# Performance work log

Hardware: AMD Instinct MI355X
Metric: run time of the kernel (lower is better)

Reference implementation:

```python
import jax, jax.numpy as jnp
import numpy as np

N, E, R = 50000, 1600000, 8
IN_F, HID_F, OUT_F = 128, 64, 64


def setup_inputs() -> dict:
    key = jax.random.key(0)
    ks = jax.random.split(key, 9)
    x = jax.random.normal(ks[0], (N, IN_F), dtype=jnp.float32)
    edge_index = jax.random.randint(ks[1], (2, E), 0, N, dtype=jnp.int64)
    edge_type = jax.random.randint(ks[2], (E,), 0, R, dtype=jnp.int64)
    # layer 1 params (scaled like glorot)
    s1 = 1.0 / np.sqrt(IN_F)
    W1_rel = jax.random.normal(ks[3], (R, IN_F, HID_F), dtype=jnp.float32) * s1
    W1_root = jax.random.normal(ks[4], (IN_F, HID_F), dtype=jnp.float32) * s1
    b1 = jnp.zeros((HID_F,), dtype=jnp.float32)
    # layer 2 params
    s2 = 1.0 / np.sqrt(HID_F)
    W2_rel = jax.random.normal(ks[5], (R, HID_F, OUT_F), dtype=jnp.float32) * s2
    W2_root = jax.random.normal(ks[6], (HID_F, OUT_F), dtype=jnp.float32) * s2
    b2 = jnp.zeros((OUT_F,), dtype=jnp.float32)
    return {"x": x, "edge_index": edge_index, "edge_type": edge_type,
            "W1_rel": W1_rel, "W1_root": W1_root, "b1": b1,
            "W2_rel": W2_rel, "W2_root": W2_root, "b2": b2}


def _rgcn_conv(x, src, dst, etype, W_rel, W_root, b):
    """PyG RGCNConv: root transform + per-relation mean-aggregated messages."""
    n = x.shape[0]
    r = W_rel.shape[0]
    # per-relation transform of all node features: [R, N, H]
    xw = jnp.einsum('nd,rdh->rnh', x, W_rel)
    # per-edge message: transformed source feature under the edge's relation
    msg = xw[etype, src]  # [E, H]
    # mean normalization per (dst, relation) pair
    key = dst * r + etype  # [E]
    cnt = jax.ops.segment_sum(jnp.ones(etype.shape, dtype=x.dtype), key,
                              num_segments=n * r)
    inv = 1.0 / jnp.maximum(cnt, 1.0)
    msg = msg * inv[key][:, None]
    # scatter-add into target nodes
    agg = jax.ops.segment_sum(msg, dst, num_segments=n)  # [N, H]
    return agg + x @ W_root + b


def reference(x, edge_index, edge_type, W1_rel, W1_root, b1, W2_rel, W2_root, b2):
    src, dst = edge_index[0], edge_index[1]
    h = _rgcn_conv(x, src, dst, edge_type, W1_rel, W1_root, b1)
    h = jax.nn.relu(h)
    out = _rgcn_conv(h, src, dst, edge_type, W2_rel, W2_root, b2)
    return out
```

## Files before the change

kernel.cpp:

```cpp
#include <hip/hip_runtime.h>


constexpr int NN  = 50000;
constexpr int NE  = 1600000;
constexpr int NR  = 8;
constexpr int FIN = 128;
constexpr int FH  = 64;

constexpr int BSH = 7;
constexpr int BN  = 1 << BSH;
constexpr int NB  = (NN + BN - 1) >> BSH;
constexpr int CAP = 6144;
constexpr int CH  = 4096;
constexpr int NAPP = (NE + CH - 1) / CH;
constexpr unsigned XWMAX = (unsigned)(NN - 1) * (NR * 64) + (NR - 1) * 64;
constexpr int K2  = 576;
constexpr int K2P = 584;

typedef __attribute__((ext_vector_type(8))) short bf16x8;
typedef __attribute__((ext_vector_type(4))) float f32x4;

__device__ __forceinline__ unsigned short f2bf(float f) {
  unsigned u = __float_as_uint(f);
  u = (u + 0x7fff + ((u >> 16) & 1)) >> 16;
  return (unsigned short)u;
}
__device__ __forceinline__ float bf2f(unsigned short b) {
  return __uint_as_float(((unsigned)b) << 16);
}
__device__ __forceinline__ bool edge_ok(unsigned s, unsigned d, unsigned r) {
  return s < NN && d < NN && r < NR;
}

__device__ void append_body(char* smem, int bx,
                            const int* __restrict__ src,
                            const int* __restrict__ dst,
                            const int* __restrict__ et,
                            int* __restrict__ bcur,
                            unsigned* __restrict__ brecs) {
  uint2* stage = (uint2*)smem;
  int* h     = (int*)(smem + (size_t)CH * 8);
  int* gbase = h + NB;
  int* sbase = gbase + NB;
  int* scur  = sbase + NB;
  int* wtot  = scur + NB;

  const int t  = threadIdx.x;
  const int c0 = bx * CH;
  const int m  = min(CH, NE - c0);

  for (int i = t; i < NB; i += 256) h[i] = 0;
  __syncthreads();

  for (int i = t; i < m; i += 256) {
    const unsigned s = (unsigned)src[c0 + i];
    const unsigned d = (unsigned)dst[c0 + i];
    const unsigned r = (unsigned)et[c0 + i];
    if (edge_ok(s, d, r)) atomicAdd(&h[d >> BSH], 1);
  }
  __syncthreads();

  const int v0 = (2 * t < NB) ? h[2 * t] : 0;
  const int v1 = (2 * t + 1 < NB) ? h[2 * t + 1] : 0;
  if (2 * t < NB     && v0) gbase[2 * t]     = atomicAdd(&bcur[2 * t], v0);
  if (2 * t + 1 < NB && v1) gbase[2 * t + 1] = atomicAdd(&bcur[2 * t + 1], v1);
  const int s = v0 + v1;
  int incl = s;
#pragma unroll
  for (int o = 1; o < 64; o <<= 1) {
    int u = __shfl_up(incl, o, 64);
    if ((t & 63) >= o) incl += u;
  }
  if ((t & 63) == 63) wtot[t >> 6] = incl;
  __syncthreads();
  int wo = 0;
  for (int w = 0; w < (t >> 6); ++w) wo += wtot[w];
  const int e = wo + incl - s;
  if (2 * t < NB)     { sbase[2 * t] = e;          scur[2 * t] = e; }
  if (2 * t + 1 < NB) { sbase[2 * t + 1] = e + v0; scur[2 * t + 1] = e + v0; }
  __syncthreads();

  for (int i = t; i < m; i += 256) {
    const unsigned sv = (unsigned)src[c0 + i];
    const unsigned d  = (unsigned)dst[c0 + i];
    const unsigned r  = (unsigned)et[c0 + i];
    if (edge_ok(sv, d, r)) {
      const int p = atomicAdd(&scur[d >> BSH], 1);
      if (p < CH) stage[p] = make_uint2((sv << 10) | (((unsigned)d & (BN - 1)) << 3) | r, d);
    }
  }
  __syncthreads();

  const int M = min(sbase[NB - 1] + h[NB - 1], CH);
  for (int j = t; j < M; j += 256) {
    const uint2 rec = stage[j];
    const int b = (int)(rec.y >> BSH);
    const int idx = min(gbase[b] + (j - sbase[b]), NB * CAP - 1);
    brecs[idx] = rec.x;
  }
}

__global__ void __launch_bounds__(256) bucket_finalize(
    const int* __restrict__ bcur, const unsigned* __restrict__ brecs,
    int* __restrict__ row_start, int* __restrict__ deg,
    unsigned* __restrict__ recs, unsigned* __restrict__ segs) {
  const int b    = blockIdx.x;
  const int base = b * CAP;
  const int m    = min(bcur[b] - base, CAP);
  const int d0   = b << BSH;
  __shared__ int cnt[BN * NR];
  __shared__ int curs[BN * NR];
  __shared__ int wtot[4];
  const int t = threadIdx.x;

  for (int i = t; i < BN * NR; i += 256) cnt[i] = 0;
  __syncthreads();
  for (int i = t; i < m; i += 256) {
    const unsigned rec = brecs[base + i];
    const int dl = (int)((rec >> 3) & (BN - 1));
    const int r  = (int)(rec & 7);
    atomicAdd(&cnt[dl * NR + r], 1);
  }
  __syncthreads();

  const int c0 = cnt[t * 4], c1 = cnt[t * 4 + 1], c2 = cnt[t * 4 + 2], c3 = cnt[t * 4 + 3];
  const int s = c0 + c1 + c2 + c3;
  int incl = s;
#pragma unroll
  for (int o = 1; o < 64; o <<= 1) {
    int u = __shfl_up(incl, o, 64);
    if ((t & 63) >= o) incl += u;
  }
  if ((t & 63) == 63) wtot[t >> 6] = incl;
  __syncthreads();
  int wo = 0;
  for (int w = 0; w < (t >> 6); ++w) wo += wtot[w];
  const int e = wo + incl - s;
  curs[t * 4]     = e;
  curs[t * 4 + 1] = e + c0;
  curs[t * 4 + 2] = e + c0 + c1;
  curs[t * 4 + 3] = e + c0 + c1 + c2;
  __syncthreads();

  if (t < BN) {
    const int d = d0 + t;
    if (d < NN) {
      const int start = curs[t * NR];
      const int end   = (t == BN - 1) ? m : curs[(t + 1) * NR];
      row_start[d] = base + start;
      deg[d]       = end - start;
#pragma unroll
      for (int r = 0; r < NR; ++r) {
        const unsigned st = (unsigned)(base + curs[t * NR + r]);
        const unsigned cn = (unsigned)min(cnt[t * NR + r], 255);
        segs[(size_t)d * NR + r] = (st << 8) | cn;
      }
    }
  }
  __syncthreads();

  for (int i = t; i < m; i += 256) {
    const unsigned rec = brecs[base + i];
    const int dl = (int)((rec >> 3) & (BN - 1));
    const int r  = (int)(rec & 7);
    const unsigned sv = rec >> 10;
    const int p  = atomicAdd(&curs[dl * NR + r], 1);
    const unsigned cn = (unsigned)min(cnt[dl * NR + r], 127);
    recs[base + min(p, CAP - 1)] = (cn << 25) | (sv << 9) | ((unsigned)r << 6);
  }
}

__global__ void prep(const float* __restrict__ W1r, const float* __restrict__ W1o,
                     const float* __restrict__ W2r, const float* __restrict__ W2o,
                     unsigned short* __restrict__ Wt1,
                     unsigned short* __restrict__ Wt2b,
                     int* __restrict__ bcur) {
  const int i  = blockIdx.x * blockDim.x + threadIdx.x;
  if (i < NB) bcur[i] = i * CAP;
  const int n1 = (NR + 1) * 64 * FIN;
  const int n2 = 64 * K2;
  if (i < n1) {
    const int g = i / (64 * FIN), rem = i % (64 * FIN);
    const int n = rem / FIN, k = rem % FIN;
    const float* W = (g < NR) ? (W1r + (size_t)g * FIN * 64) : W1o;
    Wt1[i] = f2bf(W[k * 64 + n]);
  } else if (i < n1 + n2) {
    const int j = i - n1;
    const int n = j / K2, c = j % K2;
    float v;
    if (c < 512) {
      const int r = c >> 6, kk = c & 63;
      v = W2r[((size_t)r * 64 + kk) * 64 + n];
    } else {
      const int kk = c - 512;
      v = W2o[(size_t)kk * 64 + n];
    }
    Wt2b[j] = f2bf(v);
  }
}

template <int K, bool A_FP32>
__device__ void gemm_body(char* smem, int bx,
                          const void* __restrict__ Av,
                          const unsigned short* __restrict__ Wt,
                          const float* __restrict__ bias,
                          unsigned short* __restrict__ xw,
                          float* __restrict__ root_out) {
  constexpr int KP  = K + 8;
  constexpr int NCH = 64 * (K / 8) / 256;
  constexpr int NKC = K / 32;
  unsigned short* Bs0 = (unsigned short*)smem;
  const int n0  = bx * 64;
  const int tid = threadIdx.x;
  const int wave = tid >> 6, lane = tid & 63;
  const int i16 = lane & 15, quad = lane >> 4;
  const int r0 = wave * 16 + i16;
  const int arow = n0 + r0;

  bf16x8 afrag[NKC];
  if constexpr (A_FP32) {
    const float* A = (const float*)Av;
#pragma unroll
    for (int kc = 0; kc < NKC; ++kc) {
      bf16x8 v = {};
      if (arow < NN) {
        const float* p = A + (size_t)arow * K + kc * 32 + quad * 8;
        const float4 f0 = *(const float4*)p;
        const float4 f1 = *(const float4*)(p + 4);
        v[0] = f2bf(f0.x); v[1] = f2bf(f0.y); v[2] = f2bf(f0.z); v[3] = f2bf(f0.w);
        v[4] = f2bf(f1.x); v[5] = f2bf(f1.y); v[6] = f2bf(f1.z); v[7] = f2bf(f1.w);
      }
      afrag[kc] = v;
    }
  } else {
    const unsigned short* A = (const unsigned short*)Av;
#pragma unroll
    for (int kc = 0; kc < NKC; ++kc) {
      bf16x8 v = {};
      if (arow < NN) v = *(const bf16x8*)(A + (size_t)arow * K + kc * 32 + quad * 8);
      afrag[kc] = v;
    }
  }

  for (int c = 0; c < NCH; ++c) {
    const int idx = tid + c * 256;
    const int row = idx / (K / 8), kp = (idx % (K / 8)) * 8;
    *(bf16x8*)(Bs0 + row * KP + kp) = *(const bf16x8*)(Wt + idx * 8);
  }
  __syncthreads();

  for (int g = 0; g <= NR; ++g) {
    const int buf = g & 1;
    unsigned short* Bc = Bs0 + buf * 64 * KP;
    unsigned short* Bn = Bs0 + (buf ^ 1) * 64 * KP;
    bf16x8 breg[NCH];
    if (g < NR) {
      const unsigned short* Wn = Wt + (size_t)(g + 1) * 64 * K;
#pragma unroll
      for (int c = 0; c < NCH; ++c) breg[c] = *(const bf16x8*)(Wn + (tid + c * 256) * 8);
    }

    f32x4 acc[4] = {};
#pragma unroll
    for (int kc = 0; kc < NKC; ++kc) {
      const int k0 = kc * 32 + quad * 8;
      const bf16x8 a0 = afrag[kc];
      const bf16x8 b0 = *(const bf16x8*)(Bc + (i16)      * KP + k0);
      const bf16x8 b1 = *(const bf16x8*)(Bc + (i16 + 16) * KP + k0);
      const bf16x8 b2 = *(const bf16x8*)(Bc + (i16 + 32) * KP + k0);
      const bf16x8 b3 = *(const bf16x8*)(Bc + (i16 + 48) * KP + k0);
      acc[0] = __builtin_amdgcn_mfma_f32_16x16x32_bf16(a0, b0, acc[0], 0, 0, 0);
      acc[1] = __builtin_amdgcn_mfma_f32_16x16x32_bf16(a0, b1, acc[1], 0, 0, 0);
      acc[2] = __builtin_amdgcn_mfma_f32_16x16x32_bf16(a0, b2, acc[2], 0, 0, 0);
      acc[3] = __builtin_amdgcn_mfma_f32_16x16x32_bf16(a0, b3, acc[3], 0, 0, 0);
    }

    if (g < NR) {
#pragma unroll
      for (int c = 0; c < NCH; ++c) {
        const int idx = tid + c * 256;
        const int row = idx / (K / 8), kp = (idx % (K / 8)) * 8;
        *(bf16x8*)(Bn + row * KP + kp) = breg[c];
      }
#pragma unroll
      for (int reg = 0; reg < 4; ++reg) {
        const int n = n0 + wave * 16 + quad * 4 + reg;
        if (n >= NN) continue;
        unsigned short* p = xw + (size_t)n * (NR * 64) + g * 64 + i16;
#pragma unroll
        for (int ct = 0; ct < 4; ++ct) p[ct * 16] = f2bf(acc[ct][reg]);
      }
    } else {
      float bv[4];
#pragma unroll
      for (int ct = 0; ct < 4; ++ct) bv[ct] = bias[ct * 16 + i16];
#pragma unroll
      for (int reg = 0; reg < 4; ++reg) {
        const int n = n0 + wave * 16 + quad * 4 + reg;
        if (n >= NN) continue;
        float* p = root_out + (size_t)n * 64 + i16;
#pragma unroll
        for (int ct = 0; ct < 4; ++ct) p[ct * 16] = acc[ct][reg] + bv[ct];
      }
    }
    __syncthreads();
  }
}

__global__ void __launch_bounds__(256) fused_append_gemm1(
    const int* __restrict__ src, const int* __restrict__ dst,
    const int* __restrict__ et, int* __restrict__ bcur,
    unsigned* __restrict__ brecs,
    const float* __restrict__ A, const unsigned short* __restrict__ Wt,
    const float* __restrict__ bias, unsigned short* __restrict__ xw,
    float* __restrict__ root_out) {
  extern __shared__ char smem[];
  const int bx = (int)blockIdx.x;
  if (bx % 3 == 2 && bx / 3 < NAPP)
    append_body(smem, bx / 3, src, dst, et, bcur, brecs);
  else
    gemm_body<FIN, true>(smem, bx - (bx + 1) / 3, A, Wt, bias, xw, root_out);
}

__global__ void __launch_bounds__(256) agg1(
    const int* __restrict__ row_start, const int* __restrict__ deg,
    const unsigned* __restrict__ recs, const unsigned short* __restrict__ xw,
    const float* __restrict__ root, unsigned short* __restrict__ out_b16) {
  const int gid  = blockIdx.x * blockDim.x + threadIdx.x;
  const int lane = gid & 63;
  const int d    = gid >> 6;
  if (d >= NN) return;
  const int e  = lane >> 3;
  const int l8 = lane & 7;
  const int base = row_start[d];
  const int n    = deg[d];
  const unsigned* po = recs + base;
  const unsigned short* xp = xw + l8 * 8;
  float a[8] = {};

  int i0 = 0;
  for (; i0 + 32 < n; i0 += 64) {
    unsigned rr[8];
#pragma unroll
    for (int sl = 0; sl < 8; ++sl) {
      const int i = i0 + e + 8 * sl;
      rr[sl] = (i < n) ? po[i] : 0u;
    }
    bf16x8 vv[8];
#pragma unroll
    for (int sl = 0; sl < 8; ++sl) {
      const unsigned u = min(rr[sl] & 0x01FFFFFFu, XWMAX);
      vv[sl] = *(const bf16x8*)(xp + u);
    }
#pragma unroll
    for (int sl = 0; sl < 8; ++sl) {
      float w = __builtin_amdgcn_rcpf((float)(rr[sl] >> 25));
      if (i0 + e + 8 * sl >= n) w = 0.f;
#pragma unroll
      for (int q = 0; q < 8; ++q) a[q] += bf2f((unsigned short)vv[sl][q]) * w;
    }
  }
  if (i0 < n) {
    unsigned rr[4];
#pragma unroll
    for (int sl = 0; sl < 4; ++sl) {
      const int i = i0 + e + 8 * sl;
      rr[sl] = (i < n) ? po[i] : 0u;
    }
    bf16x8 vv[4];
#pragma unroll
    for (int sl = 0; sl < 4; ++sl) {
      const unsigned u = min(rr[sl] & 0x01FFFFFFu, XWMAX);
      vv[sl] = *(const bf16x8*)(xp + u);
    }
#pragma unroll
    for (int sl = 0; sl < 4; ++sl) {
      float w = __builtin_amdgcn_rcpf((float)(rr[sl] >> 25));
      if (i0 + e + 8 * sl >= n) w = 0.f;
#pragma unroll
      for (int q = 0; q < 8; ++q) a[q] += bf2f((unsigned short)vv[sl][q]) * w;
    }
  }

#pragma unroll
  for (int q = 0; q < 8; ++q) {
    a[q] += __shfl_xor(a[q], 8, 64);
    a[q] += __shfl_xor(a[q], 16, 64);
    a[q] += __shfl_xor(a[q], 32, 64);
  }

  if (e == 0) {
    const float4 r0 = *(const float4*)(root + (size_t)d * 64 + l8 * 8);
    const float4 r1 = *(const float4*)(root + (size_t)d * 64 + l8 * 8 + 4);
    const float o[8] = {r0.x + a[0], r0.y + a[1], r0.z + a[2], r0.w + a[3],
                        r1.x + a[4], r1.y + a[5], r1.z + a[6], r1.w + a[7]};
    bf16x8 ov;
#pragma unroll
    for (int q = 0; q < 8; ++q) ov[q] = (short)f2bf(fmaxf(o[q], 0.f));
    *(bf16x8*)(out_b16 + (size_t)d * 64 + l8 * 8) = ov;
  }
}

__global__ void __launch_bounds__(256) agg2_sums(
    const unsigned* __restrict__ segs, const unsigned* __restrict__ recs,
    const unsigned short* __restrict__ hb, unsigned short* __restrict__ sums) {
  const int gid  = blockIdx.x * blockDim.x + threadIdx.x;
  const int lane = gid & 63;
  const int d    = gid >> 6;
  if (d >= NN) return;
  const int r  = lane >> 3;
  const int l8 = lane & 7;
  const unsigned sg = segs[(size_t)d * NR + r];
  const int start = (int)(sg >> 8);
  const int len   = (int)(sg & 255u);
  const unsigned* po = recs + start;
  const unsigned short* hp = hb + l8 * 8;
  float a[8] = {};

  for (int j = 0; j < len; j += 4) {
    unsigned rr[4];
#pragma unroll
    for (int sl = 0; sl < 4; ++sl)
      rr[sl] = (j + sl < len) ? po[j + sl] : 0u;
    bf16x8 vv[4];
#pragma unroll
    for (int sl = 0; sl < 4; ++sl) {
      const unsigned sv = (rr[sl] >> 9) & 0xFFFFu;
      vv[sl] = *(const bf16x8*)(hp + sv * 64);
    }
#pragma unroll
    for (int sl = 0; sl < 4; ++sl) {
      const float wk = (j + sl < len) ? 1.f : 0.f;
#pragma unroll
      for (int q = 0; q < 8; ++q) a[q] += bf2f((unsigned short)vv[sl][q]) * wk;
    }
  }

  const float w = (len > 0) ? __builtin_amdgcn_rcpf((float)len) : 0.f;
  bf16x8 ov;
#pragma unroll
  for (int q = 0; q < 8; ++q) ov[q] = (short)f2bf(a[q] * w);
  *(bf16x8*)(sums + (size_t)d * K2 + r * 64 + l8 * 8) = ov;

  if (lane < 8) {
    const bf16x8 hv = *(const bf16x8*)(hb + (size_t)d * 64 + lane * 8);
    *(bf16x8*)(sums + (size_t)d * K2 + 512 + lane * 8) = hv;
  }
}

__global__ void __launch_bounds__(256) gemm_final(
    const unsigned short* __restrict__ A,
    const unsigned short* __restrict__ Wt,
    const float* __restrict__ bias, float* __restrict__ out) {
  __shared__ unsigned short Bs[64 * K2P];
  const int tid = threadIdx.x;
  const int wave = tid >> 6, lane = tid & 63;
  const int i16 = lane & 15, quad = lane >> 4;
  const int n0 = (int)blockIdx.x * 64;
  const int node = n0 + wave * 16 + i16;

#pragma unroll
  for (int c = 0; c < 18; ++c) {
    const int idx = tid + c * 256;
    const int row = idx / 72, kp = (idx % 72) * 8;
    *(bf16x8*)(Bs + row * K2P + kp) = *(const bf16x8*)(Wt + idx * 8);
  }

  bf16x8 afrag[18];
#pragma unroll
  for (int kc = 0; kc < 18; ++kc) {
    bf16x8 v = {};
    if (node < NN) v = *(const bf16x8*)(A + (size_t)node * K2 + kc * 32 + quad * 8);
    afrag[kc] = v;
  }
  __syncthreads();

  f32x4 acc[4] = {};
#pragma unroll
  for (int kc = 0; kc < 18; ++kc) {
    const int k0 = kc * 32 + quad * 8;
    const bf16x8 a0 = afrag[kc];
    const bf16x8 b0 = *(const bf16x8*)(Bs + (i16)      * K2P + k0);
    const bf16x8 b1 = *(const bf16x8*)(Bs + (i16 + 16) * K2P + k0);
    const bf16x8 b2 = *(const bf16x8*)(Bs + (i16 + 32) * K2P + k0);
    const bf16x8 b3 = *(const bf16x8*)(Bs + (i16 + 48) * K2P + k0);
    acc[0] = __builtin_amdgcn_mfma_f32_16x16x32_bf16(b0, a0, acc[0], 0, 0, 0);
    acc[1] = __builtin_amdgcn_mfma_f32_16x16x32_bf16(b1, a0, acc[1], 0, 0, 0);
    acc[2] = __builtin_amdgcn_mfma_f32_16x16x32_bf16(b2, a0, acc[2], 0, 0, 0);
    acc[3] = __builtin_amdgcn_mfma_f32_16x16x32_bf16(b3, a0, acc[3], 0, 0, 0);
  }

  if (node < NN) {
#pragma unroll
    for (int ct = 0; ct < 4; ++ct) {
      const float4 bv = *(const float4*)(bias + ct * 16 + quad * 4);
      float* p = out + (size_t)node * 64 + ct * 16 + quad * 4;
      *(float4*)p = make_float4(acc[ct][0] + bv.x, acc[ct][1] + bv.y,
                                acc[ct][2] + bv.z, acc[ct][3] + bv.w);
    }
  }
}

extern "C" void kernel_launch(void* const* d_in, const int* in_sizes, int n_in,
                              void* d_out, int out_size, void* d_ws, size_t ws_size,
                              hipStream_t stream) {
  const float* x   = (const float*)d_in[0];
  const int*   ei  = (const int*)d_in[1];
  const int*   et  = (const int*)d_in[2];
  const float* W1r = (const float*)d_in[3];
  const float* W1o = (const float*)d_in[4];
  const float* b1  = (const float*)d_in[5];
  const float* W2r = (const float*)d_in[6];
  const float* W2o = (const float*)d_in[7];
  const float* b2  = (const float*)d_in[8];
  float* out = (float*)d_out;

  const int* src = ei;
  const int* dst = ei + NE;

  char* ws = (char*)d_ws;
  size_t off = 0;
  auto alloc = [&](size_t bytes) {
    void* p = ws + off; off += (bytes + 255) & ~(size_t)255; return p;
  };
  int*   bcur      = (int*)alloc((size_t)NB * 4);
  int*   row_start = (int*)alloc((size_t)NN * 4);
  int*   deg       = (int*)alloc((size_t)NN * 4);
  unsigned* segs   = (unsigned*)alloc((size_t)NN * NR * 4);
  unsigned* brecs  = (unsigned*)alloc((size_t)NB * CAP * 4);
  unsigned* recs   = (unsigned*)alloc((size_t)NB * CAP * 4);
  unsigned short* xw    = (unsigned short*)alloc((size_t)NN * NR * 64 * 2);
  unsigned short* hb    = (unsigned short*)alloc((size_t)NN * FH * 2);
  float*          hroot = (float*)alloc((size_t)NN * 64 * 4);
  unsigned short* sums  = (unsigned short*)alloc((size_t)NN * K2 * 2);
  unsigned short* Wt1   = (unsigned short*)alloc((size_t)(NR + 1) * 64 * FIN * 2);
  unsigned short* Wt2b  = (unsigned short*)alloc((size_t)64 * K2 * 2);

  const int nprep = (NR + 1) * 64 * FIN + 64 * K2;
  prep<<<(nprep + 255) / 256, 256, 0, stream>>>(W1r, W1o, W2r, W2o, Wt1, Wt2b, bcur);

  const int gemm_blocks = (NN + 63) / 64;
  const int agg_blocks  = (NN * 64 + 255) / 256;
  constexpr int SM1 = CH * 8 + 4 * NB * 4 + 16;

  fused_append_gemm1<<<NAPP + gemm_blocks, 256, SM1, stream>>>(
      src, dst, et, bcur, brecs, x, Wt1, b1, xw, hroot);
  bucket_finalize<<<NB, 256, 0, stream>>>(bcur, brecs, row_start, deg, recs, segs);

  agg1<<<agg_blocks, 256, 0, stream>>>(row_start, deg, recs, xw, hroot, hb);
  agg2_sums<<<agg_blocks, 256, 0, stream>>>(segs, recs, hb, sums);
  gemm_final<<<gemm_blocks, 256, 0, stream>>>(sums, Wt2b, b2, out);
}
```

Before: 242.5 us.

## Fuse layer-2 per-relation aggregation with final GEMM via shared memory

Merges the agg2_sums and gemm_final kernels into one. Each block aggregates per-relation mean messages for its 64 nodes straight into shared memory, then runs the MFMA GEMM from LDS, reading weights directly from global memory. This removes the write and reread of the intermediate sums buffer and one kernel launch. In exchange, each block does far less parallel gather work (one wave loops over 16 nodes in sequence), which lowers occupancy and latency hiding for the irregular gathers.

```diff
diff --git a/kernel.cpp b/kernel.cpp
--- a/kernel.cpp
+++ b/kernel.cpp
@@ -401,89 +401,70 @@
   }
 }
 
-__global__ void __launch_bounds__(256) agg2_sums(
+__global__ void __launch_bounds__(256) agg2_gemm(
     const unsigned* __restrict__ segs, const unsigned* __restrict__ recs,
-    const unsigned short* __restrict__ hb, unsigned short* __restrict__ sums) {
-  const int gid  = blockIdx.x * blockDim.x + threadIdx.x;
-  const int lane = gid & 63;
-  const int d    = gid >> 6;
-  if (d >= NN) return;
-  const int r  = lane >> 3;
-  const int l8 = lane & 7;
-  const unsigned sg = segs[(size_t)d * NR + r];
-  const int start = (int)(sg >> 8);
-  const int len   = (int)(sg & 255u);
-  const unsigned* po = recs + start;
-  const unsigned short* hp = hb + l8 * 8;
-  float a[8] = {};
-
-  for (int j = 0; j < len; j += 4) {
-    unsigned rr[4];
-#pragma unroll
-    for (int sl = 0; sl < 4; ++sl)
-      rr[sl] = (j + sl < len) ? po[j + sl] : 0u;
-    bf16x8 vv[4];
-#pragma unroll
-    for (int sl = 0; sl < 4; ++sl) {
-      const unsigned sv = (rr[sl] >> 9) & 0xFFFFu;
-      vv[sl] = *(const bf16x8*)(hp + sv * 64);
-    }
-#pragma unroll
-    for (int sl = 0; sl < 4; ++sl) {
-      const float wk = (j + sl < len) ? 1.f : 0.f;
-#pragma unroll
-      for (int q = 0; q < 8; ++q) a[q] += bf2f((unsigned short)vv[sl][q]) * wk;
-    }
-  }
-
-  const float w = (len > 0) ? __builtin_amdgcn_rcpf((float)len) : 0.f;
-  bf16x8 ov;
-#pragma unroll
-  for (int q = 0; q < 8; ++q) ov[q] = (short)f2bf(a[q] * w);
-  *(bf16x8*)(sums + (size_t)d * K2 + r * 64 + l8 * 8) = ov;
-
-  if (lane < 8) {
-    const bf16x8 hv = *(const bf16x8*)(hb + (size_t)d * 64 + lane * 8);
-    *(bf16x8*)(sums + (size_t)d * K2 + 512 + lane * 8) = hv;
-  }
-}
-
-__global__ void __launch_bounds__(256) gemm_final(
-    const unsigned short* __restrict__ A,
+    const unsigned short* __restrict__ hb,
     const unsigned short* __restrict__ Wt,
     const float* __restrict__ bias, float* __restrict__ out) {
-  __shared__ unsigned short Bs[64 * K2P];
+  __shared__ unsigned short Ss[64 * K2P];
   const int tid = threadIdx.x;
   const int wave = tid >> 6, lane = tid & 63;
+  const int r = lane >> 3, l8 = lane & 7;
+  const int n0 = (int)blockIdx.x * 64;
+
+  for (int j = 0; j < 16; ++j) {
+    const int row = wave * 16 + j;
+    const int d = n0 + row;
+    bf16x8 ov = {};
+    bf16x8 hv = {};
+    if (d < NN) {
+      const unsigned sg = segs[(size_t)d * NR + r];
+      const int start = (int)(sg >> 8);
+      const int len   = (int)(sg & 255u);
+      const unsigned* po = recs + start;
+      const unsigned short* hp = hb + l8 * 8;
+      float a[8] = {};
+      for (int jj = 0; jj < len; jj += 4) {
+        unsigned rr[4];
+#pragma unroll
+        for (int sl = 0; sl < 4; ++sl)
+          rr[sl] = (jj + sl < len) ? po[jj + sl] : 0u;
+        bf16x8 vv[4];
+#pragma unroll
+        for (int sl = 0; sl < 4; ++sl) {
+          const unsigned sv = (rr[sl] >> 9) & 0xFFFFu;
+          vv[sl] = *(const bf16x8*)(hp + sv * 64);
+        }
+#pragma unroll
+        for (int sl = 0; sl < 4; ++sl) {
+          const float wk = (jj + sl < len) ? 1.f : 0.f;
+#pragma unroll
+          for (int q = 0; q < 8; ++q) a[q] += bf2f((unsigned short)vv[sl][q]) * wk;
+        }
+      }
+      const float w = (len > 0) ? __builtin_amdgcn_rcpf((float)len) : 0.f;
+#pragma unroll
+      for (int q = 0; q < 8; ++q) ov[q] = (short)f2bf(a[q] * w);
+      if (r == 0) hv = *(const bf16x8*)(hb + (size_t)d * 64 + l8 * 8);
+    }
+    *(bf16x8*)(Ss + row * K2P + r * 64 + l8 * 8) = ov;
+    if (r == 0) *(bf16x8*)(Ss + row * K2P + 512 + l8 * 8) = hv;
+  }
+  __syncthreads();
+
   const int i16 = lane & 15, quad = lane >> 4;
-  const int n0 = (int)blockIdx.x * 64;
   const int node = n0 + wave * 16 + i16;
-
-#pragma unroll
-  for (int c = 0; c < 18; ++c) {
-    const int idx = tid + c * 256;
-    const int row = idx / 72, kp = (idx % 72) * 8;
-    *(bf16x8*)(Bs + row * K2P + kp) = *(const bf16x8*)(Wt + idx * 8);
-  }
-
-  bf16x8 afrag[18];
-#pragma unroll
-  for (int kc = 0; kc < 18; ++kc) {
-    bf16x8 v = {};
-    if (node < NN) v = *(const bf16x8*)(A + (size_t)node * K2 + kc * 32 + quad * 8);
-    afrag[kc] = v;
-  }
-  __syncthreads();
+  const unsigned short* As = Ss + (wave * 16 + i16) * K2P;
 
   f32x4 acc[4] = {};
 #pragma unroll
   for (int kc = 0; kc < 18; ++kc) {
     const int k0 = kc * 32 + quad * 8;
-    const bf16x8 a0 = afrag[kc];
-    const bf16x8 b0 = *(const bf16x8*)(Bs + (i16)      * K2P + k0);
-    const bf16x8 b1 = *(const bf16x8*)(Bs + (i16 + 16) * K2P + k0);
-    const bf16x8 b2 = *(const bf16x8*)(Bs + (i16 + 32) * K2P + k0);
-    const bf16x8 b3 = *(const bf16x8*)(Bs + (i16 + 48) * K2P + k0);
+    const bf16x8 a0 = *(const bf16x8*)(As + k0);
+    const bf16x8 b0 = *(const bf16x8*)(Wt + (size_t)(i16)      * K2 + k0);
+    const bf16x8 b1 = *(const bf16x8*)(Wt + (size_t)(i16 + 16) * K2 + k0);
+    const bf16x8 b2 = *(const bf16x8*)(Wt + (size_t)(i16 + 32) * K2 + k0);
+    const bf16x8 b3 = *(const bf16x8*)(Wt + (size_t)(i16 + 48) * K2 + k0);
     acc[0] = __builtin_amdgcn_mfma_f32_16x16x32_bf16(b0, a0, acc[0], 0, 0, 0);
     acc[1] = __builtin_amdgcn_mfma_f32_16x16x32_bf16(b1, a0, acc[1], 0, 0, 0);
     acc[2] = __builtin_amdgcn_mfma_f32_16x16x32_bf16(b2, a0, acc[2], 0, 0, 0);
@@ -532,7 +513,6 @@
   unsigned short* xw    = (unsigned short*)alloc((size_t)NN * NR * 64 * 2);
   unsigned short* hb    = (unsigned short*)alloc((size_t)NN * FH * 2);
   float*          hroot = (float*)alloc((size_t)NN * 64 * 4);
-  unsigned short* sums  = (unsigned short*)alloc((size_t)NN * K2 * 2);
   unsigned short* Wt1   = (unsigned short*)alloc((size_t)(NR + 1) * 64 * FIN * 2);
   unsigned short* Wt2b  = (unsigned short*)alloc((size_t)64 * K2 * 2);
 
@@ -548,6 +528,5 @@
   bucket_finalize<<<NB, 256, 0, stream>>>(bcur, brecs, row_start, deg, recs, segs);
 
   agg1<<<agg_blocks, 256, 0, stream>>>(row_start, deg, recs, xw, hroot, hb);
-  agg2_sums<<<agg_blocks, 256, 0, stream>>>(segs, recs, hb, sums);
-  gemm_final<<<gemm_blocks, 256, 0, stream>>>(sums, Wt2b, b2, out);
-}
+  agg2_gemm<<<gemm_blocks, 256, 0, stream>>>(segs, recs, hb, Wt2b, b2, out);
+}
```

Result: slower. 308.9 us (+27.4%).
